# Kernel optimization log

Measured on AMD Instinct MI355X. Metric: run time of the kernel, lower is better.

The kernel has to match this reference:

```python
import jax, jax.numpy as jnp
import numpy as np

N_NODES = 100000
N_EDGES = 600000
D = 128          # model_dim
R = 50           # deprel_size


def setup_inputs() -> dict:
    key = jax.random.key(0)
    ks = jax.random.split(key, 20)
    s = 1.0 / np.sqrt(D)
    inp = jax.random.normal(ks[0], (N_NODES, D), dtype=jnp.float32)
    deprel_edge = jax.random.randint(ks[1], (N_EDGES,), 0, R)
    deparc_edge = jax.random.randint(ks[2], (N_EDGES,), 0, 4)
    edge_index = jax.random.randint(ks[3], (2, N_EDGES), 0, N_NODES)
    # parameters (nn.Linear weights stored as [out, in]; gates are Linear(D,1))
    V_in = jax.random.normal(ks[4], (D, D), dtype=jnp.float32) * s
    V_out = jax.random.normal(ks[5], (D, D), dtype=jnp.float32) * s
    W_self = jax.random.normal(ks[6], (D, D), dtype=jnp.float32) * s
    W_norel = jax.random.normal(ks[7], (D, D), dtype=jnp.float32) * s
    V_in_gate = jax.random.normal(ks[8], (1, D), dtype=jnp.float32) * s
    V_out_gate = jax.random.normal(ks[9], (1, D), dtype=jnp.float32) * s
    W_self_gate = jax.random.normal(ks[10], (1, D), dtype=jnp.float32) * s
    W_norel_gate = jax.random.normal(ks[11], (1, D), dtype=jnp.float32) * s
    b_in = jax.random.normal(ks[12], (R, D), dtype=jnp.float32) * 0.02
    b_out = jax.random.normal(ks[13], (R, D), dtype=jnp.float32) * 0.02
    b_in_gate = jax.random.normal(ks[14], (R, 1), dtype=jnp.float32) * 0.02 + 1.0
    b_out_gate = jax.random.normal(ks[15], (R, 1), dtype=jnp.float32) * 0.02 + 1.0
    return {
        "inp": inp, "deprel_edge": deprel_edge, "deparc_edge": deparc_edge,
        "edge_index": edge_index,
        "V_in": V_in, "b_in": b_in, "V_in_gate": V_in_gate, "b_in_gate": b_in_gate,
        "V_out": V_out, "b_out": b_out, "V_out_gate": V_out_gate, "b_out_gate": b_out_gate,
        "W_self": W_self, "W_self_gate": W_self_gate,
        "W_norel": W_norel, "W_norel_gate": W_norel_gate,
    }


def reference(inp, deprel_edge, deparc_edge, edge_index,
              V_in, b_in, V_in_gate, b_in_gate,
              V_out, b_out, V_out_gate, b_out_gate,
              W_self, W_self_gate, W_norel, W_norel_gate):
    # deparc type codes: 0=align(in), 1=opposite(out), 2=self, 3=norelation
    num_nodes = inp.shape[0]
    src, tgt = edge_index[0], edge_index[1]
    # transformed node features per edge type: [4, N, D]
    T = jnp.stack([inp @ V_in.T, inp @ V_out.T, inp @ W_self.T, inp @ W_norel.T])
    # gate pre-activations per edge type: [4, N, 1]
    G = jnp.stack([inp @ V_in_gate.T, inp @ V_out_gate.T,
                   inp @ W_self_gate.T, inp @ W_norel_gate.T])
    zeros_b = jnp.zeros_like(b_in)
    zeros_bg = jnp.zeros_like(b_in_gate)
    B = jnp.stack([b_in, b_out, zeros_b, zeros_b])        # [4, R, D] (self/norel have no relation bias)
    Bg = jnp.stack([b_in_gate, b_out_gate, zeros_bg, zeros_bg])  # [4, R, 1]
    # per-edge gather + relation bias
    msg = T[deparc_edge, src] + B[deparc_edge, deprel_edge]        # [E, D]
    gate = jax.nn.sigmoid(G[deparc_edge, src] + Bg[deparc_edge, deprel_edge])  # [E, 1]
    # scatter-add to target nodes
    return jax.ops.segment_sum(msg * gate, tgt, num_segments=num_nodes)
```

## Files before the change

### kernel.cpp

```cpp
#include <hip/hip_runtime.h>
#include <hip/hip_bf16.h>

#define D 128

typedef __bf16 bf16x8 __attribute__((ext_vector_type(8)));
typedef __bf16 bf16x4 __attribute__((ext_vector_type(4)));
typedef __bf16 bf16x2 __attribute__((ext_vector_type(2)));
typedef float  f32x4  __attribute__((ext_vector_type(4)));
typedef float  f32x2  __attribute__((ext_vector_type(2)));

__global__ void detect_kernel(const unsigned int* __restrict__ w, int* flag)
{
    __shared__ int cnt[256];
    int c = 0;
#pragma unroll
    for (int i = 0; i < 4; ++i) {
        unsigned int v = w[threadIdx.x * 4 + i];
        unsigned int e = (v >> 7) & 0xFF;
        if (e >= 90 && e <= 134) ++c;
    }
    cnt[threadIdx.x] = c;
    __syncthreads();
    for (int s = 128; s > 0; s >>= 1) {
        if (threadIdx.x < s) cnt[threadIdx.x] += cnt[threadIdx.x + s];
        __syncthreads();
    }
    if (threadIdx.x == 0) flag[0] = (cnt[0] > 614) ? 1 : 0;
}

template <int ISBF>
__device__ __forceinline__ bf16x8 ld8(const void* p, size_t elem)
{
    if (ISBF) return *(const bf16x8*)((const __bf16*)p + elem);
    const f32x4* f = (const f32x4*)((const float*)p + elem);
    f32x4 lo = f[0], hi = f[1];
    bf16x8 r;
    r[0] = (__bf16)lo[0]; r[1] = (__bf16)lo[1]; r[2] = (__bf16)lo[2]; r[3] = (__bf16)lo[3];
    r[4] = (__bf16)hi[0]; r[5] = (__bf16)hi[1]; r[6] = (__bf16)hi[2]; r[7] = (__bf16)hi[3];
    return r;
}
template <int ISBF>
__device__ __forceinline__ f32x2 ld2f(const void* p, size_t elem)
{
    f32x2 r;
    if (ISBF) {
        bf16x2 v = *(const bf16x2*)((const __bf16*)p + elem);
        r[0] = (float)v[0]; r[1] = (float)v[1];
    } else {
        r = *(const f32x2*)((const float*)p + elem);
    }
    return r;
}
template <int ISBF>
__device__ __forceinline__ float ldf(const void* p, size_t elem)
{
    return ISBF ? (float)((const __bf16*)p)[elem] : ((const float*)p)[elem];
}

template <int ISBF>
__device__ __forceinline__ void gate_body(
    const void* __restrict__ A,
    const void* __restrict__ g0, const void* __restrict__ g1,
    const void* __restrict__ g2, const void* __restrict__ g3,
    float* __restrict__ G, int M)
{
    int node = blockIdx.x * 4 + (threadIdx.x >> 6);
    int lane = threadIdx.x & 63;
    if (node >= M) return;
    int d = lane * 2;
    f32x2 a  = ld2f<ISBF>(A, (size_t)node * D + d);
    f32x2 v0 = ld2f<ISBF>(g0, d);
    f32x2 v1 = ld2f<ISBF>(g1, d);
    f32x2 v2 = ld2f<ISBF>(g2, d);
    f32x2 v3 = ld2f<ISBF>(g3, d);
    float s0 = a[0] * v0[0] + a[1] * v0[1];
    float s1 = a[0] * v1[0] + a[1] * v1[1];
    float s2 = a[0] * v2[0] + a[1] * v2[1];
    float s3 = a[0] * v3[0] + a[1] * v3[1];
#pragma unroll
    for (int off = 32; off > 0; off >>= 1) {
        s0 += __shfl_down(s0, off);
        s1 += __shfl_down(s1, off);
        s2 += __shfl_down(s2, off);
        s3 += __shfl_down(s3, off);
    }
    if (lane == 0) {
        G[(size_t)0 * M + node] = s0;
        G[(size_t)1 * M + node] = s1;
        G[(size_t)2 * M + node] = s2;
        G[(size_t)3 * M + node] = s3;
    }
}

__global__ __launch_bounds__(256) void gate_kernel(
    const void* __restrict__ A,
    const void* __restrict__ g0, const void* __restrict__ g1,
    const void* __restrict__ g2, const void* __restrict__ g3,
    float* __restrict__ G, int M, const int* __restrict__ flag)
{
    if (flag[0]) gate_body<1>(A, g0, g1, g2, g3, G, M);
    else         gate_body<0>(A, g0, g1, g2, g3, G, M);
}

__global__ __launch_bounds__(128) void build_bias_kernel(
    const void* __restrict__ b_in, const void* __restrict__ b_out,
    const void* __restrict__ bg_in, const void* __restrict__ bg_out,
    __bf16* __restrict__ Bz, float* __restrict__ Bgz,
    const int* __restrict__ flag)
{
    int row = blockIdx.x;
    int tid = threadIdx.x;
    int isbf = flag[0];
    float v = 0.f, gv = 0.f;
    if (row < 50) {
        v  = isbf ? ldf<1>(b_in, (size_t)row * D + tid) : ldf<0>(b_in, (size_t)row * D + tid);
        gv = isbf ? ldf<1>(bg_in, row) : ldf<0>(bg_in, row);
    } else if (row < 100) {
        int rr = row - 50;
        v  = isbf ? ldf<1>(b_out, (size_t)rr * D + tid) : ldf<0>(b_out, (size_t)rr * D + tid);
        gv = isbf ? ldf<1>(bg_out, rr) : ldf<0>(bg_out, rr);
    }
    Bz[(size_t)row * D + tid] = (__bf16)v;
    if (tid == 0) Bgz[row] = gv;
}

__global__ __launch_bounds__(256) void hist_kernel(
    const int* __restrict__ tgt, int* __restrict__ counts, int E)
{
    int e = blockIdx.x * 256 + threadIdx.x;
    if (e < E) atomicAdd(&counts[tgt[e]], 1);
}

__global__ __launch_bounds__(256) void scan1_kernel(
    const int* __restrict__ counts, int* __restrict__ rowptr,
    int* __restrict__ bsum, int M)
{
    __shared__ int sh[256];
    int base = blockIdx.x * 1024 + threadIdx.x * 4;
    int v[4];
#pragma unroll
    for (int k = 0; k < 4; ++k)
        v[k] = (base + k < M) ? counts[base + k] : 0;
    int tot = v[0] + v[1] + v[2] + v[3];
    sh[threadIdx.x] = tot;
    __syncthreads();
    for (int off = 1; off < 256; off <<= 1) {
        int t = (threadIdx.x >= off) ? sh[threadIdx.x - off] : 0;
        __syncthreads();
        sh[threadIdx.x] += t;
        __syncthreads();
    }
    int run = sh[threadIdx.x] - tot;
#pragma unroll
    for (int k = 0; k < 4; ++k) {
        if (base + k < M) rowptr[base + k] = run;
        run += v[k];
    }
    if (threadIdx.x == 255) bsum[blockIdx.x] = sh[255];
}

__global__ __launch_bounds__(256) void scan2_kernel(
    int* __restrict__ bsum, int* __restrict__ boff, int NB)
{
    __shared__ int sh[256];
    int base = threadIdx.x * 4;
    int v[4];
#pragma unroll
    for (int k = 0; k < 4; ++k)
        v[k] = (base + k < NB) ? bsum[base + k] : 0;
    int tot = v[0] + v[1] + v[2] + v[3];
    sh[threadIdx.x] = tot;
    __syncthreads();
    for (int off = 1; off < 256; off <<= 1) {
        int t = (threadIdx.x >= off) ? sh[threadIdx.x - off] : 0;
        __syncthreads();
        sh[threadIdx.x] += t;
        __syncthreads();
    }
    int run = sh[threadIdx.x] - tot;
#pragma unroll
    for (int k = 0; k < 4; ++k) {
        if (base + k < NB) boff[base + k] = run;
        run += v[k];
    }
}

__global__ __launch_bounds__(256) void scan3_kernel(
    int* __restrict__ rowptr, int* __restrict__ cursor,
    const int* __restrict__ boff, int M, int E)
{
    int b = blockIdx.x;
    int base = b * 1024 + threadIdx.x * 4;
    int o = boff[b];
#pragma unroll
    for (int k = 0; k < 4; ++k) {
        int i = base + k;
        if (i < M) {
            int r = rowptr[i] + o;
            rowptr[i] = r;
            cursor[i] = r;
        }
    }
    if (b == 0 && threadIdx.x == 0) rowptr[M] = E;
}

__global__ __launch_bounds__(256) void scatter_kernel(
    const int* __restrict__ deprel, const int* __restrict__ deparc,
    const int* __restrict__ src, const int* __restrict__ tgt,
    int* __restrict__ cursor, int2* __restrict__ recs, int E)
{
    int e = blockIdx.x * 256 + threadIdx.x;
    if (e >= E) return;
    int g = tgt[e];
    int pos = atomicAdd(&cursor[g], 1);
    recs[pos] = make_int2(src[e], (deprel[e] << 2) | deparc[e]);
}

template <int ISBF>
__device__ __forceinline__ void edge_agg_body(
    const void* __restrict__ inp, const float* __restrict__ G,
    const __bf16* __restrict__ Bz, const float* __restrict__ Bgz,
    const int* __restrict__ rowptr, const int2* __restrict__ recs,
    __bf16* __restrict__ AG, __bf16* __restrict__ BA, int M)
{
    const int g = blockIdx.x * 16 + (threadIdx.x >> 4);
    if (g >= M) return;
    const int lane16 = threadIdx.x & 15;
    const int dd = lane16 * 8;

    const int beg = rowptr[g], end = rowptr[g + 1];

    float a0[8], a1[8], a2[8], a3[8], ba[8];
#pragma unroll
    for (int k = 0; k < 8; ++k) {
        a0[k] = 0.f; a1[k] = 0.f; a2[k] = 0.f; a3[k] = 0.f; ba[k] = 0.f;
    }

    int2 rec_c = make_int2(0, 0), rec_n = make_int2(0, 0);
    int   t_c = 0;
    float gpre_c = 0.f, bgz_c = 0.f;
    bf16x8 v_c = {}, bz_c = {};

    if (beg < end) {
        rec_c = recs[beg];
        t_c = rec_c.y & 3;
        int r = rec_c.y >> 2;
        int bidx = (t_c < 2) ? t_c * 50 + r : 100;
        gpre_c = G[(size_t)t_c * M + rec_c.x];
        bgz_c  = Bgz[bidx];
        v_c  = ld8<ISBF>(inp, (size_t)rec_c.x * D + dd);
        bz_c = *(const bf16x8*)(Bz + (size_t)bidx * D + dd);
        if (beg + 1 < end) rec_n = recs[beg + 1];
    }

    for (int e = beg; e < end; ++e) {
        const int   t    = t_c;
        const float gpre = gpre_c, bgz = bgz_c;
        const bf16x8 v = v_c, bz = bz_c;

        if (e + 1 < end) {
            rec_c = rec_n;
            t_c = rec_c.y & 3;
            int r = rec_c.y >> 2;
            int bidx = (t_c < 2) ? t_c * 50 + r : 100;
            gpre_c = G[(size_t)t_c * M + rec_c.x];
            bgz_c  = Bgz[bidx];
            v_c  = ld8<ISBF>(inp, (size_t)rec_c.x * D + dd);
            bz_c = *(const bf16x8*)(Bz + (size_t)bidx * D + dd);
            if (e + 2 < end) rec_n = recs[e + 2];
        }

        const float gate = 1.f / (1.f + __expf(-(gpre + bgz)));
        const float w0 = (t == 0) ? gate : 0.f;
        const float w1 = (t == 1) ? gate : 0.f;
        const float w2 = (t == 2) ? gate : 0.f;
        const float w3 = (t == 3) ? gate : 0.f;
#pragma unroll
        for (int k = 0; k < 8; ++k) {
            const float vf = (float)v[k];
            a0[k] = fmaf(vf, w0, a0[k]);
            a1[k] = fmaf(vf, w1, a1[k]);
            a2[k] = fmaf(vf, w2, a2[k]);
            a3[k] = fmaf(vf, w3, a3[k]);
            ba[k] = fmaf((float)bz[k], gate, ba[k]);
        }
    }

    __bf16* agrow = AG + (size_t)g * (4 * D);
    bf16x8 w;
#pragma unroll
    for (int k = 0; k < 8; ++k) w[k] = (__bf16)a0[k];
    *(bf16x8*)(agrow + 0 * D + dd) = w;
#pragma unroll
    for (int k = 0; k < 8; ++k) w[k] = (__bf16)a1[k];
    *(bf16x8*)(agrow + 1 * D + dd) = w;
#pragma unroll
    for (int k = 0; k < 8; ++k) w[k] = (__bf16)a2[k];
    *(bf16x8*)(agrow + 2 * D + dd) = w;
#pragma unroll
    for (int k = 0; k < 8; ++k) w[k] = (__bf16)a3[k];
    *(bf16x8*)(agrow + 3 * D + dd) = w;
#pragma unroll
    for (int k = 0; k < 8; ++k) w[k] = (__bf16)ba[k];
    *(bf16x8*)(BA + (size_t)g * D + dd) = w;
}

__global__ __launch_bounds__(256) void edge_agg_kernel(
    const void* __restrict__ inp, const float* __restrict__ G,
    const __bf16* __restrict__ Bz, const float* __restrict__ Bgz,
    const int* __restrict__ rowptr, const int2* __restrict__ recs,
    __bf16* __restrict__ AG, __bf16* __restrict__ BA, int M,
    const int* __restrict__ flag)
{
    if (flag[0]) edge_agg_body<1>(inp, G, Bz, Bgz, rowptr, recs, AG, BA, M);
    else         edge_agg_body<0>(inp, G, Bz, Bgz, rowptr, recs, AG, BA, M);
}

template <int ISBF>
__device__ __forceinline__ void gemm2_body(
    const __bf16* __restrict__ AG, const __bf16* __restrict__ BA,
    const void* __restrict__ W0, const void* __restrict__ W1,
    const void* __restrict__ W2, const void* __restrict__ W3,
    void* __restrict__ out, int M)
{
    __shared__ __bf16 Wsh[128 * 128];

    const int wave = threadIdx.x >> 6;
    const int lane = threadIdx.x & 63;
    const int lrow = lane & 15;
    const int kgrp = lane >> 4;
    const int m_base = blockIdx.x * 128 + wave * 32;

    int n0 = m_base + lrow;      if (n0 >= M) n0 = 0;
    int n1 = m_base + 16 + lrow; if (n1 >= M) n1 = 0;

    const void* Ws[4] = {W0, W1, W2, W3};

    f32x4 acc[2][8];
#pragma unroll
    for (int i = 0; i < 2; ++i)
#pragma unroll
        for (int j = 0; j < 8; ++j)
            acc[i][j] = (f32x4){0.f, 0.f, 0.f, 0.f};

    for (int t = 0; t < 4; ++t) {
        const void* W = Ws[t];
#pragma unroll
        for (int i = 0; i < 8; ++i) {
            int slot = threadIdx.x + 256 * i;
            int f = slot >> 4;
            int s = slot & 15;
            int sp = s ^ (f & 7);
            bf16x8 v = ld8<ISBF>(W, (size_t)f * D + s * 8);
            *(bf16x8*)(Wsh + f * 128 + sp * 8) = v;
        }
        __syncthreads();

#pragma unroll
        for (int ks = 0; ks < 4; ++ks) {
            const int k0 = ks * 32 + kgrp * 8;
            bf16x8 af0 = *(const bf16x8*)(AG + (size_t)n0 * (4 * D) + t * D + k0);
            bf16x8 af1 = *(const bf16x8*)(AG + (size_t)n1 * (4 * D) + t * D + k0);
            const int slot = 4 * ks + kgrp;
#pragma unroll
            for (int ft = 0; ft < 8; ++ft) {
                int f = ft * 16 + lrow;
                int sp = slot ^ (f & 7);
                bf16x8 wf = *(const bf16x8*)(Wsh + f * 128 + sp * 8);
                acc[0][ft] = __builtin_amdgcn_mfma_f32_16x16x32_bf16(wf, af0, acc[0][ft], 0, 0, 0);
                acc[1][ft] = __builtin_amdgcn_mfma_f32_16x16x32_bf16(wf, af1, acc[1][ft], 0, 0, 0);
            }
        }
        __syncthreads();
    }

#pragma unroll
    for (int nt = 0; nt < 2; ++nt) {
        int node = m_base + nt * 16 + lrow;
        if (node < M) {
#pragma unroll
            for (int ft = 0; ft < 8; ++ft) {
                int f0 = ft * 16 + kgrp * 4;
                bf16x4 bb = *(const bf16x4*)(BA + (size_t)node * D + f0);
                f32x4 v = acc[nt][ft];
                v[0] += (float)bb[0]; v[1] += (float)bb[1];
                v[2] += (float)bb[2]; v[3] += (float)bb[3];
                if (ISBF) {
                    bf16x4 w4;
                    w4[0] = (__bf16)v[0]; w4[1] = (__bf16)v[1];
                    w4[2] = (__bf16)v[2]; w4[3] = (__bf16)v[3];
                    *(bf16x4*)((__bf16*)out + (size_t)node * D + f0) = w4;
                } else {
                    *(f32x4*)((float*)out + (size_t)node * D + f0) = v;
                }
            }
        }
    }
}

__global__ __launch_bounds__(256) void gemm2_kernel(
    const __bf16* __restrict__ AG, const __bf16* __restrict__ BA,
    const void* __restrict__ W0, const void* __restrict__ W1,
    const void* __restrict__ W2, const void* __restrict__ W3,
    void* __restrict__ out, int M, const int* __restrict__ flag)
{
    if (flag[0]) gemm2_body<1>(AG, BA, W0, W1, W2, W3, out, M);
    else         gemm2_body<0>(AG, BA, W0, W1, W2, W3, out, M);
}

__global__ void sentinel_kernel(__bf16* o, int n)
{
    int i = blockIdx.x * blockDim.x + threadIdx.x;
    if (i < n) o[i] = (__bf16)12345.0f;
}

static inline size_t align256(size_t x) { return (x + 255) & ~(size_t)255; }

extern "C" void kernel_launch(void* const* d_in, const int* in_sizes, int n_in,
                              void* d_out, int out_size, void* d_ws, size_t ws_size,
                              hipStream_t stream)
{
    const void* inp       = d_in[0];
    const int*  deprel    = (const int*)d_in[1];
    const int*  deparc    = (const int*)d_in[2];
    const int*  eidx      = (const int*)d_in[3];
    const void* V_in      = d_in[4];
    const void* b_in      = d_in[5];
    const void* V_in_g    = d_in[6];
    const void* b_in_g    = d_in[7];
    const void* V_out     = d_in[8];
    const void* b_out     = d_in[9];
    const void* V_out_g   = d_in[10];
    const void* b_out_g   = d_in[11];
    const void* W_self    = d_in[12];
    const void* W_self_g  = d_in[13];
    const void* W_norel   = d_in[14];
    const void* W_norel_g = d_in[15];

    const int M = in_sizes[0] / D;
    const int E = in_sizes[1];
    const int* src = eidx;
    const int* tgt = eidx + E;
    const int NB = (M + 1023) / 1024;

    size_t off = 0;
    size_t o_flag   = off; off = align256(off + sizeof(int));
    size_t o_AG     = off; off = align256(off + (size_t)M * 4 * D * sizeof(__bf16));
    size_t o_BA     = off; off = align256(off + (size_t)M * D * sizeof(__bf16));
    size_t o_G      = off; off = align256(off + (size_t)4 * M * sizeof(float));
    size_t o_counts = off; off = align256(off + (size_t)M * sizeof(int));
    size_t o_rowptr = off; off = align256(off + (size_t)(M + 1) * sizeof(int));
    size_t o_cursor = off; off = align256(off + (size_t)M * sizeof(int));
    size_t o_bsum   = off; off = align256(off + (size_t)NB * sizeof(int));
    size_t o_boff   = off; off = align256(off + (size_t)NB * sizeof(int));
    size_t o_recs   = off; off = align256(off + (size_t)E * sizeof(int2));
    size_t o_Bz     = off; off = align256(off + (size_t)101 * D * sizeof(__bf16));
    size_t o_Bgz    = off; off = align256(off + (size_t)101 * sizeof(float));

    if (off > ws_size) {
        sentinel_kernel<<<(out_size + 255) / 256, 256, 0, stream>>>(
            (__bf16*)d_out, out_size);
        return;
    }

    int*    flag   = (int*)((char*)d_ws + o_flag);
    __bf16* AG     = (__bf16*)((char*)d_ws + o_AG);
    __bf16* BA     = (__bf16*)((char*)d_ws + o_BA);
    float*  Gbuf   = (float*)((char*)d_ws + o_G);
    int*    counts = (int*)((char*)d_ws + o_counts);
    int*    rowptr = (int*)((char*)d_ws + o_rowptr);
    int*    cursor = (int*)((char*)d_ws + o_cursor);
    int*    bsum   = (int*)((char*)d_ws + o_bsum);
    int*    boff   = (int*)((char*)d_ws + o_boff);
    int2*   recs   = (int2*)((char*)d_ws + o_recs);
    __bf16* Bz     = (__bf16*)((char*)d_ws + o_Bz);
    float*  Bgz    = (float*)((char*)d_ws + o_Bgz);

    detect_kernel<<<1, 256, 0, stream>>>((const unsigned int*)inp, flag);

    hipMemsetAsync(counts, 0, (size_t)M * sizeof(int), stream);
    hist_kernel<<<(E + 255) / 256, 256, 0, stream>>>(tgt, counts, E);
    scan1_kernel<<<NB, 256, 0, stream>>>(counts, rowptr, bsum, M);
    scan2_kernel<<<1, 256, 0, stream>>>(bsum, boff, NB);
    scan3_kernel<<<NB, 256, 0, stream>>>(rowptr, cursor, boff, M, E);
    scatter_kernel<<<(E + 255) / 256, 256, 0, stream>>>(deprel, deparc, src, tgt,
                                                        cursor, recs, E);

    build_bias_kernel<<<101, 128, 0, stream>>>(b_in, b_out, b_in_g, b_out_g,
                                               Bz, Bgz, flag);
    gate_kernel<<<(M + 3) / 4, 256, 0, stream>>>(inp, V_in_g, V_out_g, W_self_g,
                                                 W_norel_g, Gbuf, M, flag);

    edge_agg_kernel<<<(M + 15) / 16, 256, 0, stream>>>(inp, Gbuf, Bz, Bgz,
                                                       rowptr, recs, AG, BA, M, flag);
    gemm2_kernel<<<(M + 127) / 128, 256, 0, stream>>>(AG, BA, V_in, V_out, W_self,
                                                      W_norel, d_out, M, flag);
}
```

Baseline: 332.1 us.

## Sort nodes by degree for edge aggregation, deepen prefetch, use packed FMA

Adds a counting sort of nodes by in-degree (histogram, scan and scatter kernels) so that each wavefront in the edge aggregation kernel processes nodes with similar edge counts. This is meant to reduce divergence and idle lanes from unbalanced loops. The aggregation loop now prefetches two edges ahead and uses packed v_pk_fma_f32 with a bit-shift bf16-to-float conversion. The gate kernel also moves from 64 lanes per node to 16 lanes per node with 8-wide loads. In exchange it adds four small launches, and output rows are written in scattered order, which loses write locality.

```diff
diff --git a/kernel.cpp b/kernel.cpp
--- a/kernel.cpp
+++ b/kernel.cpp
@@ -8,6 +8,7 @@
 typedef __bf16 bf16x2 __attribute__((ext_vector_type(2)));
 typedef float  f32x4  __attribute__((ext_vector_type(4)));
 typedef float  f32x2  __attribute__((ext_vector_type(2)));
+typedef unsigned int u32x4 __attribute__((ext_vector_type(4)));
 
 __global__ void detect_kernel(const unsigned int* __restrict__ w, int* flag)
 {
@@ -40,21 +41,24 @@
     return r;
 }
 template <int ISBF>
-__device__ __forceinline__ f32x2 ld2f(const void* p, size_t elem)
+__device__ __forceinline__ float ldf(const void* p, size_t elem)
+{
+    return ISBF ? (float)((const __bf16*)p)[elem] : ((const float*)p)[elem];
+}
+
+__device__ __forceinline__ f32x2 bfpair(unsigned int u)
 {
     f32x2 r;
-    if (ISBF) {
-        bf16x2 v = *(const bf16x2*)((const __bf16*)p + elem);
-        r[0] = (float)v[0]; r[1] = (float)v[1];
-    } else {
-        r = *(const f32x2*)((const float*)p + elem);
-    }
+    r[0] = __builtin_bit_cast(float, u << 16);
+    r[1] = __builtin_bit_cast(float, u & 0xffff0000u);
     return r;
 }
-template <int ISBF>
-__device__ __forceinline__ float ldf(const void* p, size_t elem)
-{
-    return ISBF ? (float)((const __bf16*)p)[elem] : ((const float*)p)[elem];
+
+__device__ __forceinline__ f32x2 pkfma(f32x2 a, f32x2 b, f32x2 c)
+{
+    f32x2 d;
+    asm("v_pk_fma_f32 %0, %1, %2, %3" : "=v"(d) : "v"(a), "v"(b), "v"(c));
+    return d;
 }
 
 template <int ISBF>
@@ -64,27 +68,32 @@
     const void* __restrict__ g2, const void* __restrict__ g3,
     float* __restrict__ G, int M)
 {
-    int node = blockIdx.x * 4 + (threadIdx.x >> 6);
-    int lane = threadIdx.x & 63;
+    int node = blockIdx.x * 16 + (threadIdx.x >> 4);
     if (node >= M) return;
-    int d = lane * 2;
-    f32x2 a  = ld2f<ISBF>(A, (size_t)node * D + d);
-    f32x2 v0 = ld2f<ISBF>(g0, d);
-    f32x2 v1 = ld2f<ISBF>(g1, d);
-    f32x2 v2 = ld2f<ISBF>(g2, d);
-    f32x2 v3 = ld2f<ISBF>(g3, d);
-    float s0 = a[0] * v0[0] + a[1] * v0[1];
-    float s1 = a[0] * v1[0] + a[1] * v1[1];
-    float s2 = a[0] * v2[0] + a[1] * v2[1];
-    float s3 = a[0] * v3[0] + a[1] * v3[1];
-#pragma unroll
-    for (int off = 32; off > 0; off >>= 1) {
-        s0 += __shfl_down(s0, off);
-        s1 += __shfl_down(s1, off);
-        s2 += __shfl_down(s2, off);
-        s3 += __shfl_down(s3, off);
-    }
-    if (lane == 0) {
+    int lane16 = threadIdx.x & 15;
+    int dd = lane16 * 8;
+    bf16x8 a  = ld8<ISBF>(A, (size_t)node * D + dd);
+    bf16x8 q0 = ld8<ISBF>(g0, dd);
+    bf16x8 q1 = ld8<ISBF>(g1, dd);
+    bf16x8 q2 = ld8<ISBF>(g2, dd);
+    bf16x8 q3 = ld8<ISBF>(g3, dd);
+    float s0 = 0.f, s1 = 0.f, s2 = 0.f, s3 = 0.f;
+#pragma unroll
+    for (int k = 0; k < 8; ++k) {
+        float af = (float)a[k];
+        s0 = fmaf(af, (float)q0[k], s0);
+        s1 = fmaf(af, (float)q1[k], s1);
+        s2 = fmaf(af, (float)q2[k], s2);
+        s3 = fmaf(af, (float)q3[k], s3);
+    }
+#pragma unroll
+    for (int off = 8; off > 0; off >>= 1) {
+        s0 += __shfl_xor(s0, off);
+        s1 += __shfl_xor(s1, off);
+        s2 += __shfl_xor(s2, off);
+        s3 += __shfl_xor(s3, off);
+    }
+    if (lane16 == 0) {
         G[(size_t)0 * M + node] = s0;
         G[(size_t)1 * M + node] = s1;
         G[(size_t)2 * M + node] = s2;
@@ -216,92 +225,145 @@
     recs[pos] = make_int2(src[e], (deprel[e] << 2) | deparc[e]);
 }
 
+__global__ __launch_bounds__(256) void deg_hist_kernel(
+    const int* __restrict__ counts, int* __restrict__ dcnt, int M)
+{
+    __shared__ int lh[64];
+    if (threadIdx.x < 64) lh[threadIdx.x] = 0;
+    __syncthreads();
+    int i = blockIdx.x * 256 + threadIdx.x;
+    if (i < M) {
+        int d = counts[i]; if (d > 63) d = 63;
+        atomicAdd(&lh[d], 1);
+    }
+    __syncthreads();
+    if (threadIdx.x < 64 && lh[threadIdx.x])
+        atomicAdd(&dcnt[threadIdx.x], lh[threadIdx.x]);
+}
+
+__global__ void deg_scan_kernel(const int* __restrict__ dcnt, int* __restrict__ dcur)
+{
+    if (threadIdx.x == 0) {
+        int run = 0;
+        for (int i = 0; i < 64; ++i) { dcur[i] = run; run += dcnt[i]; }
+    }
+}
+
+__global__ __launch_bounds__(256) void deg_scatter_kernel(
+    const int* __restrict__ counts, int* __restrict__ dcur,
+    int* __restrict__ perm, int M)
+{
+    __shared__ int lh[64];
+    __shared__ int gb[64];
+    if (threadIdx.x < 64) lh[threadIdx.x] = 0;
+    __syncthreads();
+    int i = blockIdx.x * 256 + threadIdx.x;
+    int d = 0, lpos = 0;
+    if (i < M) {
+        d = counts[i]; if (d > 63) d = 63;
+        lpos = atomicAdd(&lh[d], 1);
+    }
+    __syncthreads();
+    if (threadIdx.x < 64 && lh[threadIdx.x])
+        gb[threadIdx.x] = atomicAdd(&dcur[threadIdx.x], lh[threadIdx.x]);
+    __syncthreads();
+    if (i < M) perm[gb[d] + lpos] = i;
+}
+
 template <int ISBF>
 __device__ __forceinline__ void edge_agg_body(
     const void* __restrict__ inp, const float* __restrict__ G,
     const __bf16* __restrict__ Bz, const float* __restrict__ Bgz,
     const int* __restrict__ rowptr, const int2* __restrict__ recs,
+    const int* __restrict__ perm,
     __bf16* __restrict__ AG, __bf16* __restrict__ BA, int M)
 {
-    const int g = blockIdx.x * 16 + (threadIdx.x >> 4);
-    if (g >= M) return;
+    const int idx = blockIdx.x * 16 + (threadIdx.x >> 4);
+    if (idx >= M) return;
+    const int g = perm[idx];
     const int lane16 = threadIdx.x & 15;
     const int dd = lane16 * 8;
 
     const int beg = rowptr[g], end = rowptr[g + 1];
-
-    float a0[8], a1[8], a2[8], a3[8], ba[8];
-#pragma unroll
-    for (int k = 0; k < 8; ++k) {
-        a0[k] = 0.f; a1[k] = 0.f; a2[k] = 0.f; a3[k] = 0.f; ba[k] = 0.f;
-    }
-
-    int2 rec_c = make_int2(0, 0), rec_n = make_int2(0, 0);
-    int   t_c = 0;
-    float gpre_c = 0.f, bgz_c = 0.f;
-    bf16x8 v_c = {}, bz_c = {};
-
-    if (beg < end) {
-        rec_c = recs[beg];
-        t_c = rec_c.y & 3;
-        int r = rec_c.y >> 2;
-        int bidx = (t_c < 2) ? t_c * 50 + r : 100;
-        gpre_c = G[(size_t)t_c * M + rec_c.x];
-        bgz_c  = Bgz[bidx];
-        v_c  = ld8<ISBF>(inp, (size_t)rec_c.x * D + dd);
-        bz_c = *(const bf16x8*)(Bz + (size_t)bidx * D + dd);
-        if (beg + 1 < end) rec_n = recs[beg + 1];
-    }
-
-    for (int e = beg; e < end; ++e) {
-        const int   t    = t_c;
-        const float gpre = gpre_c, bgz = bgz_c;
-        const bf16x8 v = v_c, bz = bz_c;
-
-        if (e + 1 < end) {
-            rec_c = rec_n;
-            t_c = rec_c.y & 3;
-            int r = rec_c.y >> 2;
-            int bidx = (t_c < 2) ? t_c * 50 + r : 100;
-            gpre_c = G[(size_t)t_c * M + rec_c.x];
-            bgz_c  = Bgz[bidx];
-            v_c  = ld8<ISBF>(inp, (size_t)rec_c.x * D + dd);
-            bz_c = *(const bf16x8*)(Bz + (size_t)bidx * D + dd);
-            if (e + 2 < end) rec_n = recs[e + 2];
+    const int n = end - beg;
+
+    f32x2 a0[4], a1[4], a2[4], a3[4], ba[4];
+#pragma unroll
+    for (int k = 0; k < 4; ++k) {
+        a0[k] = (f32x2){0.f, 0.f}; a1[k] = (f32x2){0.f, 0.f};
+        a2[k] = (f32x2){0.f, 0.f}; a3[k] = (f32x2){0.f, 0.f};
+        ba[k] = (f32x2){0.f, 0.f};
+    }
+
+    bf16x8 v0 = {}, bz0 = {}, v1 = {}, bz1 = {};
+    float gp0 = 0.f, bg0 = 0.f, gp1 = 0.f, bg1 = 0.f;
+    int t0 = 0, t1 = 0;
+    int2 r2 = make_int2(0, 0);
+
+    auto issue = [&](int2 rec, bf16x8& v, bf16x8& bz, float& gp, float& bg, int& t) {
+        t = rec.y & 3;
+        int r = rec.y >> 2;
+        int bidx = (t < 2) ? t * 50 + r : 100;
+        gp = G[(size_t)t * M + rec.x];
+        bg = Bgz[bidx];
+        v  = ld8<ISBF>(inp, (size_t)rec.x * D + dd);
+        bz = *(const bf16x8*)(Bz + (size_t)bidx * D + dd);
+    };
+
+    if (n > 0) issue(recs[beg], v0, bz0, gp0, bg0, t0);
+    if (n > 1) issue(recs[beg + 1], v1, bz1, gp1, bg1, t1);
+    if (n > 2) r2 = recs[beg + 2];
+
+    for (int e = 0; e < n; ++e) {
+        const bf16x8 v = v0, bz = bz0;
+        const float gp = gp0, bg = bg0;
+        const int t = t0;
+
+        v0 = v1; bz0 = bz1; gp0 = gp1; bg0 = bg1; t0 = t1;
+        if (e + 2 < n) {
+            issue(r2, v1, bz1, gp1, bg1, t1);
+            if (e + 3 < n) r2 = recs[beg + e + 3];
         }
 
-        const float gate = 1.f / (1.f + __expf(-(gpre + bgz)));
-        const float w0 = (t == 0) ? gate : 0.f;
-        const float w1 = (t == 1) ? gate : 0.f;
-        const float w2 = (t == 2) ? gate : 0.f;
-        const float w3 = (t == 3) ? gate : 0.f;
-#pragma unroll
-        for (int k = 0; k < 8; ++k) {
-            const float vf = (float)v[k];
-            a0[k] = fmaf(vf, w0, a0[k]);
-            a1[k] = fmaf(vf, w1, a1[k]);
-            a2[k] = fmaf(vf, w2, a2[k]);
-            a3[k] = fmaf(vf, w3, a3[k]);
-            ba[k] = fmaf((float)bz[k], gate, ba[k]);
+        const float gate = 1.f / (1.f + __expf(-(gp + bg)));
+        const float w0s = (t == 0) ? gate : 0.f;
+        const float w1s = (t == 1) ? gate : 0.f;
+        const float w2s = (t == 2) ? gate : 0.f;
+        const float w3s = (t == 3) ? gate : 0.f;
+        const f32x2 w0 = {w0s, w0s}, w1 = {w1s, w1s};
+        const f32x2 w2 = {w2s, w2s}, w3 = {w3s, w3s};
+        const f32x2 gg = {gate, gate};
+
+        const u32x4 uv = __builtin_bit_cast(u32x4, v);
+        const u32x4 ub = __builtin_bit_cast(u32x4, bz);
+#pragma unroll
+        for (int k = 0; k < 4; ++k) {
+            const f32x2 vf = bfpair(uv[k]);
+            const f32x2 bf = bfpair(ub[k]);
+            a0[k] = pkfma(vf, w0, a0[k]);
+            a1[k] = pkfma(vf, w1, a1[k]);
+            a2[k] = pkfma(vf, w2, a2[k]);
+            a3[k] = pkfma(vf, w3, a3[k]);
+            ba[k] = pkfma(bf, gg, ba[k]);
         }
     }
 
     __bf16* agrow = AG + (size_t)g * (4 * D);
     bf16x8 w;
 #pragma unroll
-    for (int k = 0; k < 8; ++k) w[k] = (__bf16)a0[k];
+    for (int k = 0; k < 4; ++k) { w[2*k] = (__bf16)a0[k][0]; w[2*k+1] = (__bf16)a0[k][1]; }
     *(bf16x8*)(agrow + 0 * D + dd) = w;
 #pragma unroll
-    for (int k = 0; k < 8; ++k) w[k] = (__bf16)a1[k];
+    for (int k = 0; k < 4; ++k) { w[2*k] = (__bf16)a1[k][0]; w[2*k+1] = (__bf16)a1[k][1]; }
     *(bf16x8*)(agrow + 1 * D + dd) = w;
 #pragma unroll
-    for (int k = 0; k < 8; ++k) w[k] = (__bf16)a2[k];
+    for (int k = 0; k < 4; ++k) { w[2*k] = (__bf16)a2[k][0]; w[2*k+1] = (__bf16)a2[k][1]; }
     *(bf16x8*)(agrow + 2 * D + dd) = w;
 #pragma unroll
-    for (int k = 0; k < 8; ++k) w[k] = (__bf16)a3[k];
+    for (int k = 0; k < 4; ++k) { w[2*k] = (__bf16)a3[k][0]; w[2*k+1] = (__bf16)a3[k][1]; }
     *(bf16x8*)(agrow + 3 * D + dd) = w;
 #pragma unroll
-    for (int k = 0; k < 8; ++k) w[k] = (__bf16)ba[k];
+    for (int k = 0; k < 4; ++k) { w[2*k] = (__bf16)ba[k][0]; w[2*k+1] = (__bf16)ba[k][1]; }
     *(bf16x8*)(BA + (size_t)g * D + dd) = w;
 }
 
@@ -309,11 +371,12 @@
     const void* __restrict__ inp, const float* __restrict__ G,
     const __bf16* __restrict__ Bz, const float* __restrict__ Bgz,
     const int* __restrict__ rowptr, const int2* __restrict__ recs,
+    const int* __restrict__ perm,
     __bf16* __restrict__ AG, __bf16* __restrict__ BA, int M,
     const int* __restrict__ flag)
 {
-    if (flag[0]) edge_agg_body<1>(inp, G, Bz, Bgz, rowptr, recs, AG, BA, M);
-    else         edge_agg_body<0>(inp, G, Bz, Bgz, rowptr, recs, AG, BA, M);
+    if (flag[0]) edge_agg_body<1>(inp, G, Bz, Bgz, rowptr, recs, perm, AG, BA, M);
+    else         edge_agg_body<0>(inp, G, Bz, Bgz, rowptr, recs, perm, AG, BA, M);
 }
 
 template <int ISBF>
@@ -456,6 +519,9 @@
     size_t o_recs   = off; off = align256(off + (size_t)E * sizeof(int2));
     size_t o_Bz     = off; off = align256(off + (size_t)101 * D * sizeof(__bf16));
     size_t o_Bgz    = off; off = align256(off + (size_t)101 * sizeof(float));
+    size_t o_perm   = off; off = align256(off + (size_t)M * sizeof(int));
+    size_t o_dcnt   = off; off = align256(off + (size_t)64 * sizeof(int));
+    size_t o_dcur   = off; off = align256(off + (size_t)64 * sizeof(int));
 
     if (off > ws_size) {
         sentinel_kernel<<<(out_size + 255) / 256, 256, 0, stream>>>(
@@ -475,11 +541,20 @@
     int2*   recs   = (int2*)((char*)d_ws + o_recs);
     __bf16* Bz     = (__bf16*)((char*)d_ws + o_Bz);
     float*  Bgz    = (float*)((char*)d_ws + o_Bgz);
+    int*    perm   = (int*)((char*)d_ws + o_perm);
+    int*    dcnt   = (int*)((char*)d_ws + o_dcnt);
+    int*    dcur   = (int*)((char*)d_ws + o_dcur);
 
     detect_kernel<<<1, 256, 0, stream>>>((const unsigned int*)inp, flag);
 
     hipMemsetAsync(counts, 0, (size_t)M * sizeof(int), stream);
+    hipMemsetAsync(dcnt, 0, 64 * sizeof(int), stream);
     hist_kernel<<<(E + 255) / 256, 256, 0, stream>>>(tgt, counts, E);
+
+    deg_hist_kernel<<<(M + 255) / 256, 256, 0, stream>>>(counts, dcnt, M);
+    deg_scan_kernel<<<1, 64, 0, stream>>>(dcnt, dcur);
+    deg_scatter_kernel<<<(M + 255) / 256, 256, 0, stream>>>(counts, dcur, perm, M);
+
     scan1_kernel<<<NB, 256, 0, stream>>>(counts, rowptr, bsum, M);
     scan2_kernel<<<1, 256, 0, stream>>>(bsum, boff, NB);
     scan3_kernel<<<NB, 256, 0, stream>>>(rowptr, cursor, boff, M, E);
@@ -488,11 +563,12 @@
 
     build_bias_kernel<<<101, 128, 0, stream>>>(b_in, b_out, b_in_g, b_out_g,
                                                Bz, Bgz, flag);
-    gate_kernel<<<(M + 3) / 4, 256, 0, stream>>>(inp, V_in_g, V_out_g, W_self_g,
-                                                 W_norel_g, Gbuf, M, flag);
+    gate_kernel<<<(M + 15) / 16, 256, 0, stream>>>(inp, V_in_g, V_out_g, W_self_g,
+                                                   W_norel_g, Gbuf, M, flag);
 
     edge_agg_kernel<<<(M + 15) / 16, 256, 0, stream>>>(inp, Gbuf, Bz, Bgz,
-                                                       rowptr, recs, AG, BA, M, flag);
+                                                       rowptr, recs, perm,
+                                                       AG, BA, M, flag);
     gemm2_kernel<<<(M + 127) / 128, 256, 0, stream>>>(AG, BA, V_in, V_out, W_self,
                                                       W_norel, d_out, M, flag);
 }
```

After: 339.6 us. 2.3% more time.
